# Kernel optimization log

Hardware: AMD Instinct MI355X
Metric: run time of the kernel (lower is better)

Reference implementation:

```python
import jax, jax.numpy as jnp
import numpy as np

W = 32            # window_size
HEADS = 8
DH = 64           # dim_head
DIM = 512
NREL = 2 * W - 1  # 63
N = W * W + 1     # 1025 (cls token)
B = 32
EPS = 1e-6
SCALE = DH ** -0.5


def _bias_indices():
    r = np.arange(W)
    gx, gy = np.meshgrid(r, r, indexing='ij')
    grid = np.stack((gx.reshape(-1), gy.reshape(-1)))        # (2, w*w)
    rel = grid[:, :, None] - grid[:, None, :] + (W - 1)       # (2, n, n)
    return (rel[0] * 1 + rel[1] * NREL).astype(np.int32)      # (w*w, w*w)


def setup_inputs() -> dict:
    key = jax.random.key(0)
    ks = jax.random.split(key, 5)
    return {
        'x': jax.random.normal(ks[0], (B, N, DIM), dtype=jnp.float32),
        'w_qkv': jax.random.normal(ks[1], (DIM, 3 * HEADS * DH), dtype=jnp.float32) * 0.02,
        'g': jnp.ones((DH,), dtype=jnp.float32),                      # RMSNorm scale
        'pe_table': jax.random.normal(ks[2], (NREL * NREL, HEADS), dtype=jnp.float32) * 0.02,
        'w_out': jax.random.normal(ks[3], (HEADS * DH, DIM), dtype=jnp.float32) * 0.02,
        'b_out': jnp.zeros((DIM,), dtype=jnp.float32),
        'bias_idx': jnp.asarray(_bias_indices()),
    }


def _rmsnorm(t, g):
    return t * jax.lax.rsqrt(jnp.mean(t * t, axis=-1, keepdims=True) + EPS) * g


def reference(x, w_qkv, g, pe_table, w_out, b_out, bias_idx):
    b, n, _ = x.shape
    # qkv projection; chunk(3) on last dim == leading axis of (3, H, DH)
    qkv = (x @ w_qkv).reshape(b, n, 3, HEADS, DH)
    qkv = jnp.transpose(qkv, (2, 0, 3, 1, 4))                 # (3, b, h, n, d)
    q, k, v = qkv[0], qkv[1], qkv[2]
    dots = jnp.einsum('bhid,bhjd->bhij', _rmsnorm(q, g), _rmsnorm(k, g)) * SCALE
    bias = jnp.transpose(pe_table[bias_idx], (2, 0, 1))       # (h, w*w, w*w)
    dots = dots.at[:, :, 1:, 1:].add(bias)                    # skip cls row/col
    attn = jax.nn.softmax(dots, axis=-1)
    out = jnp.einsum('bhij,bhjd->bhid', attn, v)
    out = jnp.transpose(out, (0, 2, 1, 3)).reshape(b, n, HEADS * DH)
    return out @ w_out + b_out
```

## Files before the change

### kernel.cpp

```cpp
#include <hip/hip_runtime.h>

typedef short bf16x8 __attribute__((ext_vector_type(8)));
typedef float f32x4 __attribute__((ext_vector_type(4)));
typedef float f32x16 __attribute__((ext_vector_type(16)));
typedef unsigned int u32;
typedef u32 u32x4 __attribute__((ext_vector_type(4)));
typedef unsigned short u16;

#define B_    32
#define N_    1025
#define H_    8
#define DIM_  512
#define M_    (B_*N_)
#define QP_   1152
#define BIP_  1152
#define NT_   34
#define KVSZ_ (NT_*2048)
#define BT_   (BIP_*32)
#define SCALE_ 0.125f
#define LOG2E_ 1.4426950408889634f

#define CONVN_ (M_*DIM_/4)
#define TQKV_  (512*1536)
#define TOUT_  (512*512)
#define NBIAS_ (8*NT_*1152*32)
#define NZT_   3096576
#define PREP_TOTAL_ (CONVN_+TQKV_+TOUT_+NBIAS_+NZT_)

__device__ __forceinline__ u16 f2bf(float f){
  unsigned u = __builtin_bit_cast(unsigned, f);
  u += 0x7FFFu + ((u >> 16) & 1u);
  return (u16)(u >> 16);
}
__device__ __forceinline__ u32 cvtpk(float a, float b){
  u32 r;
  asm("v_cvt_pk_bf16_f32 %0, %1, %2" : "=v"(r) : "v"(a), "v"(b));
  return r;
}
__device__ __forceinline__ void pswap(u32 &a, u32 &b){
  asm("v_permlane32_swap_b32 %0, %1" : "+v"(a), "+v"(b));
}
__device__ __forceinline__ void gll16(const u16* g, u16* l){
  __builtin_amdgcn_global_load_lds((const __attribute__((address_space(1))) u16*)(g),
                                   (__attribute__((address_space(3))) u16*)(l), 16, 0, 0);
}

__global__ __launch_bounds__(256)
void k_prep(const float* __restrict__ x, const float* __restrict__ wqkv,
            const float* __restrict__ wout, const int* __restrict__ idx,
            const float* __restrict__ pe,
            u16* __restrict__ xb, u16* __restrict__ wT, u16* __restrict__ woT,
            u16* __restrict__ br,
            u16* __restrict__ qn, u16* __restrict__ kn2, u16* __restrict__ v2){
  int i = blockIdx.x*256 + threadIdx.x;
  if (i < CONVN_){
    float4 v = ((const float4*)x)[i];
    ushort4 r;
    r.x = f2bf(v.x); r.y = f2bf(v.y); r.z = f2bf(v.z); r.w = f2bf(v.w);
    ((ushort4*)xb)[i] = r;
  } else if (i < CONVN_+TQKV_){
    int j = i - CONVN_;
    int n = j / 512, k = j - n*512;
    wT[j] = f2bf(wqkv[k*1536 + n]);
  } else if (i < CONVN_+TQKV_+TOUT_){
    int j = i - (CONVN_+TQKV_);
    int n = j / 512, k = j - n*512;
    woT[j] = f2bf(wout[k*512 + n]);
  } else if (i < CONVN_+TQKV_+TOUT_+NBIAS_){
    int j = i - (CONVN_+TQKV_+TOUT_);
    int v = j & 15, hi = (j>>4)&1;
    int t1 = j >> 5;
    int ii = t1 % 1152;
    int t2 = t1 / 1152;
    int tj = t2 % NT_;
    int h = t2 / NT_;
    int jj = tj*32 + (v&3) + 8*(v>>2) + 4*hi;
    float val;
    if (jj >= 1 && jj <= 1024 && ii >= 1 && ii <= 1024)
      val = pe[idx[(ii-1)*1024 + (jj-1)]*8 + h] * LOG2E_;
    else
      val = (jj <= 1024) ? 0.f : -1e9f;
    br[j] = f2bf(val);
  } else {
    int j = i - (CONVN_+TQKV_+TOUT_+NBIAS_);
    if (j < 2080768){
      int bh = j / (127*64); int r = j - bh*(127*64);
      qn[((size_t)bh*QP_ + 1025 + (r>>6))*64 + (r&63)] = 0;
    } else if (j < 2588672){
      int k = j - 2080768; int bh = k/1984; int r = k - bh*1984;
      int n = 1025 + (r>>6), d = r & 63;
      kn2[(size_t)bh*KVSZ_ + 65536 + ((d>>3)<<8) + ((n&31)<<3) + (d&7)] = 0;
    } else if (j < 3096576){
      int k = j - 2588672; int bh = k/1984; int r = k - bh*1984;
      int n = 1025 + (r>>6), d = r & 63;
      v2[(size_t)bh*KVSZ_ + 65536 + (((n>>3)&3)<<9) + (d<<3) + (n&7)] = 0;
    }
  }
}

__global__ __launch_bounds__(256, 4)
void k_qkv(const u16* __restrict__ xb, const u16* __restrict__ wT, const float* __restrict__ g,
           u16* __restrict__ qn, u16* __restrict__ kn2, u16* __restrict__ v2){
  __shared__ u16 sh[16384];
  const int tid = threadIdx.x;
  const int lane = tid & 63, wid = tid >> 6;
  const int lg = lane >> 4, lr = lane & 15;
  const int wm = wid >> 1, wn = wid & 1;

  int orig = blockIdx.x;
  int xcd = orig & 7, idx = orig >> 3;
  int wgid = (xcd < 4 ? xcd*386 : 1544 + (xcd-4)*385) + idx;
  int mt = wgid / 12, nt = wgid - mt*12;
  const int m0 = mt*128, n0 = nt*128;
  const int qkv_t = nt >> 2;
  const int h = ((nt & 3) << 1) + wn;

  const int srow = tid >> 2;
  const int schunk = (tid & 3) ^ ((tid >> 3) & 3);
  const u16* asrc = xb + (size_t)(m0 + srow)*DIM_ + schunk*8;
  const u16* bsrc = wT + (size_t)(n0 + srow)*DIM_ + schunk*8;
  const int rsw = (lg ^ ((lr>>1)&3)) << 3;

  u16* As = sh;
  u16* Bs = sh + 8192;

  f32x4 acc[4][4];
#pragma unroll
  for (int m=0;m<4;++m)
#pragma unroll
    for (int n=0;n<4;++n) acc[m][n] = {0.f,0.f,0.f,0.f};

  gll16(asrc,            As + wid*512);
  gll16(asrc + 64*DIM_,  As + 2048 + wid*512);
  gll16(bsrc,            Bs + wid*512);
  gll16(bsrc + 64*DIM_,  Bs + 2048 + wid*512);

  for (int s=0; s<16; ++s){
    const int cur = s & 1;
    __syncthreads();
    if (s < 15){
      const int ko = (s+1)*32;
      gll16(asrc + ko,           As + (cur^1)*4096 + wid*512);
      gll16(asrc + ko + 64*DIM_, As + (cur^1)*4096 + 2048 + wid*512);
      gll16(bsrc + ko,           Bs + (cur^1)*4096 + wid*512);
      gll16(bsrc + ko + 64*DIM_, Bs + (cur^1)*4096 + 2048 + wid*512);
    }
    bf16x8 af[4], bf[4];
#pragma unroll
    for (int m=0;m<4;++m) af[m] = *(const bf16x8*)(As + cur*4096 + (64*wm+16*m+lr)*32 + rsw);
#pragma unroll
    for (int n=0;n<4;++n) bf[n] = *(const bf16x8*)(Bs + cur*4096 + (64*wn+16*n+lr)*32 + rsw);
    __builtin_amdgcn_s_setprio(1);
#pragma unroll
    for (int m=0;m<4;++m)
#pragma unroll
      for (int n=0;n<4;++n)
        acc[m][n] = __builtin_amdgcn_mfma_f32_16x16x32_bf16(af[m], bf[n], acc[m][n], 0, 0, 0);
    __builtin_amdgcn_s_setprio(0);
  }

  float gv[4];
#pragma unroll
  for (int n=0;n<4;++n)
    gv[n] = (qkv_t==0) ? g[16*n+lr]*(SCALE_*LOG2E_) : (qkv_t==1 ? g[16*n+lr] : 1.f);

#pragma unroll
  for (int m=0;m<4;++m){
    float rstd[4];
    if (qkv_t < 2){
#pragma unroll
      for (int r=0;r<4;++r){
        float s = 0.f;
#pragma unroll
        for (int n=0;n<4;++n) s += acc[m][n][r]*acc[m][n][r];
        s += __shfl_xor(s, 1); s += __shfl_xor(s, 2);
        s += __shfl_xor(s, 4); s += __shfl_xor(s, 8);
        rstd[r] = rsqrtf(s*(1.f/64.f) + 1e-6f);
      }
    } else {
#pragma unroll
      for (int r=0;r<4;++r) rstd[r] = 1.f;
    }
#pragma unroll
    for (int r=0;r<4;++r){
      int mg = m0 + 64*wm + 16*m + 4*lg + r;
      if (mg < M_){
        int b = mg / N_, pos = mg - b*N_;
        int bh = b*H_ + h;
#pragma unroll
        for (int n=0;n<4;++n){
          int d = 16*n + lr;
          u16 val = f2bf(acc[m][n][r]*rstd[r]*gv[n]);
          if (qkv_t == 0)
            qn[((size_t)bh*QP_ + pos)*64 + d] = val;
          else if (qkv_t == 1)
            kn2[(size_t)bh*KVSZ_ + (pos>>5)*2048 + ((d>>3)<<8) + ((pos&31)<<3) + (d&7)] = val;
          else
            v2[(size_t)bh*KVSZ_ + (pos>>5)*2048 + (((pos>>3)&3)<<9) + (d<<3) + (pos&7)] = val;
        }
      }
    }
  }
}

#define TILE(buf, off, B0, B1) do { \
  f32x16 s; \
  _Pragma("unroll") \
  for (int r=0;r<16;++r){ \
    u16 bv = (r < 8) ? ((u16)(B0)[r]) : ((u16)(B1)[r-8]); \
    s[r] = __builtin_bit_cast(float, ((u32)bv) << 16); \
  } \
  __builtin_amdgcn_s_setprio(1); \
  _Pragma("unroll") \
  for (int c=0;c<4;++c){ \
    bf16x8 kf = *(const bf16x8*)(&Ks[buf][0] + (off) + (2*c + hi)*256 + il*8); \
    s = __builtin_amdgcn_mfma_f32_32x32x16_bf16(kf, qf[c], s, 0, 0, 0); \
  } \
  __builtin_amdgcn_s_setprio(0); \
  _Pragma("unroll") \
  for (int r=0;r<16;++r) s[r] = __builtin_amdgcn_exp2f(s[r]); \
  u32 X0 = cvtpk(s[0],s[1]),   X1 = cvtpk(s[2],s[3]); \
  u32 Y0 = cvtpk(s[4],s[5]),   Y1 = cvtpk(s[6],s[7]); \
  u32 X2 = cvtpk(s[8],s[9]),   X3 = cvtpk(s[10],s[11]); \
  u32 Y2 = cvtpk(s[12],s[13]), Y3 = cvtpk(s[14],s[15]); \
  pswap(X0, Y0); pswap(X1, Y1); pswap(X2, Y2); pswap(X3, Y3); \
  u32x4 w0 = {X0, X1, Y0, Y1}; \
  u32x4 w1 = {X2, X3, Y2, Y3}; \
  bf16x8 pv0 = __builtin_bit_cast(bf16x8, w0); \
  bf16x8 pv1 = __builtin_bit_cast(bf16x8, w1); \
  __builtin_amdgcn_s_setprio(1); \
  _Pragma("unroll") \
  for (int c2=0;c2<2;++c2){ \
    bf16x8 pv = c2 ? pv1 : pv0; \
    const u16* vb = &Vs[buf][0] + (off) + (2*c2 + hi)*512; \
    bf16x8 vfA = *(const bf16x8*)(vb + il*8); \
    bf16x8 vfB = *(const bf16x8*)(vb + 256 + il*8); \
    oA = __builtin_amdgcn_mfma_f32_32x32x16_bf16(vfA, pv, oA, 0, 0, 0); \
    oB = __builtin_amdgcn_mfma_f32_32x32x16_bf16(vfB, pv, oB, 0, 0, 0); \
    oS = __builtin_amdgcn_mfma_f32_32x32x16_bf16(onesf, pv, oS, 0, 0, 0); \
  } \
  __builtin_amdgcn_s_setprio(0); \
} while(0)

__global__ __launch_bounds__(256, 3)
void k_attn2(const u16* __restrict__ qn, const u16* __restrict__ kn2, const u16* __restrict__ v2,
             const u16* __restrict__ br, u16* __restrict__ ao){
  __shared__ u16 Ks[2][4096];
  __shared__ u16 Vs[2][4096];
  const int tid = threadIdx.x;
  const int lane = tid & 63, wave = tid >> 6;
  const int il = lane & 31, hi = lane >> 5;
  int wg = ((blockIdx.x & 7) * 288) + (blockIdx.x >> 3);
  int h = wg / 288;
  int rem = wg - h*288;
  int b = rem / 9, qt = rem - (rem/9)*9;
  int bh = b*8 + h;
  int i0 = qt*128 + wave*32;
  const bool active = (i0 <= 1024);

  const u16* qp = qn + ((size_t)bh*QP_ + (i0 + il))*64 + hi*8;
  bf16x8 qf[4];
#pragma unroll
  for (int c=0;c<4;++c) qf[c] = *(const bf16x8*)(qp + 16*c);

  const u16* ksrc = kn2 + (size_t)bh*KVSZ_ + tid*8;
  const u16* vsrc = v2  + (size_t)bh*KVSZ_ + tid*8;

  gll16(ksrc,        &Ks[0][wave*512]);
  gll16(ksrc + 2048, &Ks[0][2048 + wave*512]);
  gll16(vsrc,        &Vs[0][wave*512]);
  gll16(vsrc + 2048, &Vs[0][2048 + wave*512]);

  f32x16 oA, oB, oS;
#pragma unroll
  for (int r=0;r<16;++r){ oA[r]=0.f; oB[r]=0.f; oS[r]=0.f; }

  const bf16x8 onesf = {0x3F80,0x3F80,0x3F80,0x3F80,0x3F80,0x3F80,0x3F80,0x3F80};

  const u16* bptr = br + ((size_t)(h*NT_)*BIP_ + (i0 + il))*32 + hi*16;
  bf16x8 cb0 = *(const bf16x8*)(bptr);
  bf16x8 cb1 = *(const bf16x8*)(bptr + 8);
  bf16x8 cb2 = *(const bf16x8*)(bptr + BT_);
  bf16x8 cb3 = *(const bf16x8*)(bptr + BT_ + 8);

  for (int t=0; t<16; ++t){
    const int cur = t & 1;
    __syncthreads();
    {
      const int base = (2*t+2)*2048;
      gll16(ksrc + base,        &Ks[cur^1][wave*512]);
      gll16(ksrc + base + 2048, &Ks[cur^1][2048 + wave*512]);
      gll16(vsrc + base,        &Vs[cur^1][wave*512]);
      gll16(vsrc + base + 2048, &Vs[cur^1][2048 + wave*512]);
    }
    if (active){
      TILE(cur, 0, cb0, cb1);
      cb0 = *(const bf16x8*)(bptr + 2*BT_);
      cb1 = *(const bf16x8*)(bptr + 2*BT_ + 8);
      TILE(cur, 2048, cb2, cb3);
      cb2 = *(const bf16x8*)(bptr + 3*BT_);
      cb3 = *(const bf16x8*)(bptr + 3*BT_ + 8);
      bptr += 2*BT_;
    }
  }
  __syncthreads();
  if (active){
    TILE(0, 0, cb0, cb1);
  }

  int i = i0 + il;
  if (i < N_){
    float inv = 1.f / oS[0];
    u16* op = ao + ((size_t)(b*N_ + i))*DIM_ + h*64;
#pragma unroll
    for (int q=0;q<4;++q)
#pragma unroll
      for (int pr=0;pr<2;++pr){
        int d0 = 8*q + 4*hi + 2*pr;
        u32 wA = cvtpk(oA[4*q+2*pr]*inv, oA[4*q+2*pr+1]*inv);
        u32 wB = cvtpk(oB[4*q+2*pr]*inv, oB[4*q+2*pr+1]*inv);
        *(u32*)(op + d0) = wA;
        *(u32*)(op + 32 + d0) = wB;
      }
  }
}

__global__ __launch_bounds__(256)
void k_oproj(const u16* __restrict__ ab, const u16* __restrict__ wT, const float* __restrict__ bo,
             float* __restrict__ out){
  __shared__ u16 sh[16384];
  const int tid = threadIdx.x;
  const int lane = tid & 63, wid = tid >> 6;
  const int lg = lane >> 4, lr = lane & 15;
  const int wm = wid >> 1, wn = wid & 1;

  int orig = blockIdx.x;
  int xcd = orig & 7, idx = orig >> 3;
  int wgid = (xcd < 4 ? xcd*129 : 516 + (xcd-4)*128) + idx;
  int mt = wgid >> 2, nt = wgid & 3;
  const int m0 = mt*128, n0 = nt*128;

  const int srow = tid >> 2;
  const int schunk = (tid & 3) ^ ((tid >> 3) & 3);
  const u16* asrc = ab + (size_t)(m0 + srow)*DIM_ + schunk*8;
  const u16* bsrc = wT + (size_t)(n0 + srow)*DIM_ + schunk*8;
  const int rsw = (lg ^ ((lr>>1)&3)) << 3;

  u16* As = sh;
  u16* Bs = sh + 8192;

  f32x4 acc[4][4];
#pragma unroll
  for (int m=0;m<4;++m)
#pragma unroll
    for (int n=0;n<4;++n) acc[m][n] = {0.f,0.f,0.f,0.f};

  gll16(asrc,            As + wid*512);
  gll16(asrc + 64*DIM_,  As + 2048 + wid*512);
  gll16(bsrc,            Bs + wid*512);
  gll16(bsrc + 64*DIM_,  Bs + 2048 + wid*512);

  for (int s=0; s<16; ++s){
    const int cur = s & 1;
    __syncthreads();
    if (s < 15){
      const int ko = (s+1)*32;
      gll16(asrc + ko,           As + (cur^1)*4096 + wid*512);
      gll16(asrc + ko + 64*DIM_, As + (cur^1)*4096 + 2048 + wid*512);
      gll16(bsrc + ko,           Bs + (cur^1)*4096 + wid*512);
      gll16(bsrc + ko + 64*DIM_, Bs + (cur^1)*4096 + 2048 + wid*512);
    }
    bf16x8 af[4], bf[4];
#pragma unroll
    for (int m=0;m<4;++m) af[m] = *(const bf16x8*)(As + cur*4096 + (64*wm+16*m+lr)*32 + rsw);
#pragma unroll
    for (int n=0;n<4;++n) bf[n] = *(const bf16x8*)(Bs + cur*4096 + (64*wn+16*n+lr)*32 + rsw);
    __builtin_amdgcn_s_setprio(1);
#pragma unroll
    for (int m=0;m<4;++m)
#pragma unroll
      for (int n=0;n<4;++n)
        acc[m][n] = __builtin_amdgcn_mfma_f32_16x16x32_bf16(af[m], bf[n], acc[m][n], 0, 0, 0);
    __builtin_amdgcn_s_setprio(0);
  }

  float bb[4];
#pragma unroll
  for (int n=0;n<4;++n) bb[n] = bo[n0 + 64*wn + 16*n + lr];
#pragma unroll
  for (int m=0;m<4;++m)
#pragma unroll
    for (int r=0;r<4;++r){
      int mg = m0 + 64*wm + 16*m + 4*lg + r;
      if (mg < M_){
#pragma unroll
        for (int n=0;n<4;++n)
          out[(size_t)mg*DIM_ + n0 + 64*wn + 16*n + lr] = acc[m][n][r] + bb[n];
      }
    }
}

extern "C" void kernel_launch(void* const* d_in, const int* in_sizes, int n_in,
                              void* d_out, int out_size, void* d_ws, size_t ws_size,
                              hipStream_t stream) {
  const float* x     = (const float*)d_in[0];
  const float* w_qkv = (const float*)d_in[1];
  const float* g     = (const float*)d_in[2];
  const float* pe    = (const float*)d_in[3];
  const float* w_out = (const float*)d_in[4];
  const float* b_out = (const float*)d_in[5];
  const int*   bidx  = (const int*)d_in[6];
  float* out = (float*)d_out;

  char* ws = (char*)d_ws;
  u16*   xb    = (u16*)(ws);
  u16*   wT    = (u16*)(ws + 33587200);
  u16*   woT   = (u16*)(ws + 35160064);
  u16*   qnb   = (u16*)(ws + 35684352);
  u16*   kn2   = (u16*)(ws + 73433088);
  u16*   v2    = (u16*)(ws + 109084672);
  u16*   biasr = (u16*)(ws + 144736256);
  u16*   aob   = xb;

  k_prep<<<PREP_TOTAL_/256, 256, 0, stream>>>(x, w_qkv, w_out, bidx, pe,
                                              xb, wT, woT, biasr, qnb, kn2, v2);
  k_qkv<<<3084, 256, 0, stream>>>(xb, wT, g, qnb, kn2, v2);
  k_attn2<<<2304, 256, 0, stream>>>(qnb, kn2, v2, biasr, aob);
  k_oproj<<<1028, 256, 0, stream>>>(aob, woT, b_out, out);
}
```

Before: 275.6 us.

## Split lone cls-row query tile into separate split-K attention kernel

The main attention kernel previously launched 9 query tiles per (batch, head), and the ninth tile held only the single cls row, so most of its waves were idle. Now the main kernel covers exactly 8 tiles of 128 rows with power-of-two index math and no activity checks. A new small kernel handles row 1024 per (batch, head) by spreading the key tiles across 4 waves and reducing partial outputs and row sums through shared memory. This removes 256 mostly idle workgroups and their full K/V sweeps, at the cost of an extra launch and a serialized tail kernel.

```diff
diff --git a/kernel.cpp b/kernel.cpp
--- a/kernel.cpp
+++ b/kernel.cpp
@@ -250,13 +250,12 @@
   const int tid = threadIdx.x;
   const int lane = tid & 63, wave = tid >> 6;
   const int il = lane & 31, hi = lane >> 5;
-  int wg = ((blockIdx.x & 7) * 288) + (blockIdx.x >> 3);
-  int h = wg / 288;
-  int rem = wg - h*288;
-  int b = rem / 9, qt = rem - (rem/9)*9;
+  int wg = ((blockIdx.x & 7) << 8) + (blockIdx.x >> 3);
+  int h = wg >> 8;
+  int rem = wg & 255;
+  int b = rem >> 3, qt = rem & 7;
   int bh = b*8 + h;
   int i0 = qt*128 + wave*32;
-  const bool active = (i0 <= 1024);
 
   const u16* qp = qn + ((size_t)bh*QP_ + (i0 + il))*64 + hi*8;
   bf16x8 qf[4];
@@ -293,24 +292,20 @@
       gll16(vsrc + base,        &Vs[cur^1][wave*512]);
       gll16(vsrc + base + 2048, &Vs[cur^1][2048 + wave*512]);
     }
-    if (active){
-      TILE(cur, 0, cb0, cb1);
-      cb0 = *(const bf16x8*)(bptr + 2*BT_);
-      cb1 = *(const bf16x8*)(bptr + 2*BT_ + 8);
-      TILE(cur, 2048, cb2, cb3);
-      cb2 = *(const bf16x8*)(bptr + 3*BT_);
-      cb3 = *(const bf16x8*)(bptr + 3*BT_ + 8);
-      bptr += 2*BT_;
-    }
+    TILE(cur, 0, cb0, cb1);
+    cb0 = *(const bf16x8*)(bptr + 2*BT_);
+    cb1 = *(const bf16x8*)(bptr + 2*BT_ + 8);
+    TILE(cur, 2048, cb2, cb3);
+    cb2 = *(const bf16x8*)(bptr + 3*BT_);
+    cb3 = *(const bf16x8*)(bptr + 3*BT_ + 8);
+    bptr += 2*BT_;
   }
   __syncthreads();
-  if (active){
-    TILE(0, 0, cb0, cb1);
-  }
-
-  int i = i0 + il;
-  if (i < N_){
+  TILE(0, 0, cb0, cb1);
+
+  {
     float inv = 1.f / oS[0];
+    int i = i0 + il;
     u16* op = ao + ((size_t)(b*N_ + i))*DIM_ + h*64;
 #pragma unroll
     for (int q=0;q<4;++q)
@@ -322,6 +317,82 @@
         *(u32*)(op + d0) = wA;
         *(u32*)(op + 32 + d0) = wB;
       }
+  }
+}
+
+__global__ __launch_bounds__(256)
+void k_attn_cls(const u16* __restrict__ qn, const u16* __restrict__ kn2, const u16* __restrict__ v2,
+                const u16* __restrict__ br, u16* __restrict__ ao){
+  __shared__ u16 Ks[2][8192];
+  __shared__ u16 Vs[2][8192];
+  __shared__ float red[4][2][33];
+  const int tid = threadIdx.x;
+  const int lane = tid & 63, wave = tid >> 6;
+  const int il = lane & 31, hi = lane >> 5;
+  const int bh = blockIdx.x;
+  const int b = bh >> 3, h = bh & 7;
+
+  const u16* qp = qn + ((size_t)bh*QP_ + (1024 + il))*64 + hi*8;
+  bf16x8 qf[4];
+#pragma unroll
+  for (int c=0;c<4;++c) qf[c] = *(const bf16x8*)(qp + 16*c);
+
+  const u16* ksrc = kn2 + (size_t)bh*KVSZ_ + tid*8;
+  const u16* vsrc = v2  + (size_t)bh*KVSZ_ + tid*8;
+
+#pragma unroll
+  for (int tt=0;tt<4;++tt){
+    gll16(ksrc + tt*2048, &Ks[0][tt*2048 + wave*512]);
+    gll16(vsrc + tt*2048, &Vs[0][tt*2048 + wave*512]);
+  }
+
+  f32x16 oA, oB, oS;
+#pragma unroll
+  for (int r=0;r<16;++r){ oA[r]=0.f; oB[r]=0.f; oS[r]=0.f; }
+  const bf16x8 onesf = {0x3F80,0x3F80,0x3F80,0x3F80,0x3F80,0x3F80,0x3F80,0x3F80};
+
+  for (int rr=0; rr<9; ++rr){
+    const int cur = rr & 1;
+    __syncthreads();
+    if (rr < 8){
+      const int t0n = 4*(rr+1);
+#pragma unroll
+      for (int tt=0;tt<4;++tt){
+        int t = t0n + tt;
+        if (t < NT_){
+          gll16(ksrc + t*2048, &Ks[cur^1][tt*2048 + wave*512]);
+          gll16(vsrc + t*2048, &Vs[cur^1][tt*2048 + wave*512]);
+        }
+      }
+    }
+    const int t = 4*rr + wave;
+    if (t <= 32){
+      const u16* bp2 = br + ((size_t)(h*NT_ + t)*BIP_ + (1024 + il))*32 + hi*16;
+      bf16x8 c0 = *(const bf16x8*)(bp2);
+      bf16x8 c1 = *(const bf16x8*)(bp2 + 8);
+      TILE(cur, wave*2048, c0, c1);
+    }
+  }
+
+  if (il == 0){
+#pragma unroll
+    for (int r=0;r<16;++r){
+      red[wave][hi][r]      = oA[r];
+      red[wave][hi][16 + r] = oB[r];
+    }
+    red[wave][hi][32] = oS[0];
+  }
+  __syncthreads();
+  if (tid < 64){
+    int d = tid;
+    int half = d >> 5;
+    int dd = d & 31;
+    int q = dd >> 3, h2 = (dd >> 2) & 1, pr = (dd >> 1) & 1, e = dd & 1;
+    int reg = half*16 + 4*q + 2*pr + e;
+    float v = 0.f, ls = 0.f;
+#pragma unroll
+    for (int w=0; w<4; ++w){ v += red[w][h2][reg]; ls += red[w][0][32]; }
+    ao[((size_t)(b*N_ + 1024))*DIM_ + h*64 + d] = f2bf(v / ls);
   }
 }
 
@@ -425,6 +496,7 @@
   k_prep<<<PREP_TOTAL_/256, 256, 0, stream>>>(x, w_qkv, w_out, bidx, pe,
                                               xb, wT, woT, biasr, qnb, kn2, v2);
   k_qkv<<<3084, 256, 0, stream>>>(xb, wT, g, qnb, kn2, v2);
-  k_attn2<<<2304, 256, 0, stream>>>(qnb, kn2, v2, biasr, aob);
+  k_attn2<<<2048, 256, 0, stream>>>(qnb, kn2, v2, biasr, aob);
+  k_attn_cls<<<256, 256, 0, stream>>>(qnb, kn2, v2, biasr, aob);
   k_oproj<<<1028, 256, 0, stream>>>(aob, woT, b_out, out);
 }
```

Result: slower. 282.5 us (+2.5%).
